# Performance work log

Hardware: AMD Instinct MI355X
Metric: run time of the kernel (lower is better)

The kernel has to match this reference:

```python
import jax, jax.numpy as jnp
import numpy as np

B, S, P, N, V = 8, 16, 32, 2048, 2562
K_SAMPLE = 500      # samples_per_slot
K_NEAREST = 3
MIN_DIST = 0.5
FALLOFF = 5.0
GW, SW, RW = 0.7, 0.3, 0.2


def _icosphere(level=4):
    t = (1.0 + 5.0 ** 0.5) / 2.0
    v = np.array([[-1, t, 0], [1, t, 0], [-1, -t, 0], [1, -t, 0],
                  [0, -1, t], [0, 1, t], [0, -1, -t], [0, 1, -t],
                  [t, 0, -1], [t, 0, 1], [-t, 0, -1], [-t, 0, 1]], dtype=np.float64)
    v /= np.linalg.norm(v, axis=1, keepdims=True)
    f = [[0, 11, 5], [0, 5, 1], [0, 1, 7], [0, 7, 10], [0, 10, 11],
         [1, 5, 9], [5, 11, 4], [11, 10, 2], [10, 7, 6], [7, 1, 8],
         [3, 9, 4], [3, 4, 2], [3, 2, 6], [3, 6, 8], [3, 8, 9],
         [4, 9, 5], [2, 4, 11], [6, 2, 10], [8, 6, 7], [9, 8, 1]]
    verts = [x for x in v]
    for _ in range(level):
        cache = {}
        def mid(a, b):
            key = (min(a, b), max(a, b))
            if key in cache:
                return cache[key]
            m = verts[a] + verts[b]
            m = m / np.linalg.norm(m)
            verts.append(m)
            cache[key] = len(verts) - 1
            return cache[key]
        nf = []
        for a, b, c in f:
            ab, bc, ca = mid(a, b), mid(b, c), mid(c, a)
            nf += [[a, ab, ca], [b, bc, ab], [c, ca, bc], [ab, bc, ca]]
        f = nf
    return np.asarray(verts, dtype=np.float32)


def _euler_xyz_to_matrix(ang):
    # pytorch3d euler_angles_to_matrix(..., 'XYZ'): R = Rx(a) @ Ry(b) @ Rz(c)
    a, b, c = ang[..., 0], ang[..., 1], ang[..., 2]
    ca, sa = jnp.cos(a), jnp.sin(a)
    cb, sb = jnp.cos(b), jnp.sin(b)
    cc, sc = jnp.cos(c), jnp.sin(c)
    o, z = jnp.ones_like(a), jnp.zeros_like(a)
    sh = ang.shape[:-1] + (3, 3)
    Rx = jnp.stack([o, z, z, z, ca, -sa, z, sa, ca], -1).reshape(sh)
    Ry = jnp.stack([cb, z, sb, z, o, z, -sb, z, cb], -1).reshape(sh)
    Rz = jnp.stack([cc, -sc, z, sc, cc, z, z, z, o], -1).reshape(sh)
    return Rx @ Ry @ Rz


def _cdist2(x, y):
    # squared euclidean distances: x [..., n, 3], y [..., m, 3] -> [..., n, m]
    x2 = (x * x).sum(-1)[..., :, None]
    y2 = (y * y).sum(-1)[..., None, :]
    return jnp.maximum(x2 + y2 - 2.0 * jnp.einsum('...nd,...md->...nm', x, y), 0.0)


def _forward(scales, transforms, prototype_weights, prototype_offsets, target_pcl, verts):
    # --- transform_mesh ---
    R = _euler_xyz_to_matrix(transforms[..., 3:])          # [B,S,P,3,3]
    deformed = verts[None] + prototype_offsets              # [P,V,3]
    rotated = jnp.einsum('pvj,bspij->bspvi', deformed, R)   # verts @ R^T
    scaled = rotated * scales[:, :, None, None, :]          # [B,S,P,V,3]
    translated = scaled + transforms[:, :, :, None, :3]
    final = jnp.einsum('bspvi,bsp->bsvi', translated, prototype_weights)  # [B,S,V,3]

    # --- hybrid chamfer loss ---
    pred = final[:, :, :K_SAMPLE, :]                        # deterministic per-slot samples
    pred_flat = pred.reshape(B, S * K_SAMPLE, 3)
    # global: target -> all predicted points, mean of K nearest squared dists
    d2g = _cdist2(target_pcl, pred_flat)                    # [B,N,S*K]
    knn = -jax.lax.top_k(-d2g, K_NEAREST)[0]
    global_loss = knn.mean()
    # per-slot: each slot's points -> target, nearest neighbor squared dist
    d2s = _cdist2(pred, target_pcl[:, None])                # [B,S,K,N]
    per_slot_loss = d2s.min(-1).mean()
    # centroid repulsion
    cent = final.mean(axis=2)                               # [B,S,3]
    eye = jnp.eye(S, dtype=final.dtype)
    d = jnp.sqrt(_cdist2(cent, cent) + eye)                 # eye keeps diag grads finite
    rep = jnp.exp(FALLOFF * jnp.maximum(MIN_DIST - d, 0.0)) * (1.0 - eye)
    rep_loss = (rep.sum(axis=(1, 2)) / (S * (S - 1))).mean()

    return GW * global_loss + SW * per_slot_loss + RW * rep_loss


def setup_inputs() -> dict:
    key = jax.random.key(0)
    ks = jax.random.split(key, 5)
    scales = jax.random.uniform(ks[0], (B, S, 1), jnp.float32) * 0.5 + 0.5
    transforms = jax.random.normal(ks[1], (B, S, P, 6), jnp.float32)
    w = jax.random.uniform(ks[2], (B, S, P), jnp.float32) + 1e-3
    prototype_weights = w / w.sum(-1, keepdims=True)
    prototype_offsets = jax.random.normal(ks[3], (P, V, 3), jnp.float32) * 0.1
    target_pcl = jax.random.normal(ks[4], (B, N, 3), jnp.float32)
    verts = jnp.asarray(_icosphere(4))                      # [2562,3]
    return {"scales": scales, "transforms": transforms,
            "prototype_weights": prototype_weights,
            "prototype_offsets": prototype_offsets,
            "target_pcl": target_pcl, "verts": verts}


def reference(scales, transforms, prototype_weights, prototype_offsets, target_pcl, verts):
    return _forward(scales, transforms, prototype_weights, prototype_offsets, target_pcl, verts)
```

## Files before the change

### kernel.cpp

```cpp
#include <hip/hip_runtime.h>
#include <math.h>

namespace {
constexpr int cB = 8, cS = 16, cP = 32, cN = 2048, cV = 2562;
constexpr int cK = 500;
constexpr int cJ = cS * cK;
constexpr int cJC = 16;
constexpr int cJCH = cJ / cJC;
constexpr int cNC = 8;
constexpr int cNCH = cN / cNC;
constexpr int cJPAD = 8192;
constexpr int cBN = cB * cN;
constexpr float FINF = 3.402823466e+38f;

constexpr int OFF_PRED4 = 0;
constexpr int OFF_TGT4  = 256000;
constexpr int OFF_VBAR  = 321536;
constexpr int OFF_OBAR  = 321540;
constexpr int OFF_SM    = 321664;
constexpr int OFF_SC    = 358528;
constexpr int OFF_T3    = 358912;
constexpr int OFF_PSP   = 1145344;
constexpr int OFF_GM    = 1669632;
constexpr int OFF_PS    = 1669696;
}

__device__ __forceinline__ float block_sum(float v, float* red, int tid) {
  red[tid] = v;
  __syncthreads();
  for (int s = 128; s > 0; s >>= 1) {
    if (tid < s) red[tid] += red[tid + s];
    __syncthreads();
  }
  return red[0];
}

__device__ __forceinline__ void top3_insert(float& t0, float& t1, float& t2, float d) {
  const float nt2 = fminf(t2, fmaxf(t1, d));
  const float nt1 = __builtin_amdgcn_fmed3f(t0, t1, d);
  t0 = fminf(t0, d);
  t1 = nt1;
  t2 = nt2;
}

__global__ void __launch_bounds__(256) k_front(const float* __restrict__ scales,
                                               const float* __restrict__ transforms,
                                               const float* __restrict__ pw,
                                               const float* __restrict__ offs,
                                               const float* __restrict__ verts,
                                               const float* __restrict__ target,
                                               float* __restrict__ ws) {
  const int blk = blockIdx.x;
  const int tid = threadIdx.x;
  if (blk <= cP) {
    __shared__ float red[256];
    const float* src = (blk < cP) ? (offs + blk * cV * 3) : verts;
    float acc0 = 0.f, acc1 = 0.f, acc2 = 0.f;
    for (int v = tid; v < cV; v += 256) {
      acc0 += src[v * 3 + 0];
      acc1 += src[v * 3 + 1];
      acc2 += src[v * 3 + 2];
    }
    float* dst = (blk < cP) ? (ws + OFF_OBAR + blk * 3) : (ws + OFF_VBAR);
    float a[3] = {acc0, acc1, acc2};
    for (int c = 0; c < 3; ++c) {
      float s = block_sum(a[c], red, tid);
      if (tid == 0) dst[c] = s / (float)cV;
      __syncthreads();
    }
  } else if (blk <= cP + 64) {
    const int idx = (blk - (cP + 1)) * 256 + tid;
    const float x = target[idx * 3 + 0];
    const float y = target[idx * 3 + 1];
    const float z = target[idx * 3 + 2];
    ((float4*)(ws + OFF_TGT4))[idx] =
        make_float4(x, y, z, 0.5f * fmaf(x, x, fmaf(y, y, z * z)));
  } else {
    const int bs = blk - (cP + 65);
    __shared__ float sM[cP][9];
    __shared__ float sC[3];
    __shared__ float sWT[cP][3];
    if (tid < cP) {
      const int p = tid;
      const float* t = transforms + (bs * cP + p) * 6;
      const float w = pw[bs * cP + p];
      const float sc = scales[bs];
      const float a = t[3], b = t[4], c = t[5];
      const float ca = cosf(a), sa = sinf(a);
      const float cb = cosf(b), sb = sinf(b);
      const float cg = cosf(c), sg = sinf(c);
      const float f = w * sc;
      sM[p][0] = f * (cb * cg);
      sM[p][1] = f * (-cb * sg);
      sM[p][2] = f * (sb);
      sM[p][3] = f * (ca * sg + sa * sb * cg);
      sM[p][4] = f * (ca * cg - sa * sb * sg);
      sM[p][5] = f * (-sa * cb);
      sM[p][6] = f * (sa * sg - ca * sb * cg);
      sM[p][7] = f * (sa * cg + ca * sb * sg);
      sM[p][8] = f * (ca * cb);
      sWT[p][0] = w * t[0];
      sWT[p][1] = w * t[1];
      sWT[p][2] = w * t[2];
    }
    __syncthreads();
    if (tid < 3) {
      float s = 0.f;
      for (int p = 0; p < cP; ++p) s += sWT[p][tid];
      sC[tid] = s;
    }
    __syncthreads();
    if (tid < cP * 9) ws[OFF_SM + bs * 288 + tid] = ((const float*)sM)[tid];
    if (tid < 3) ws[OFF_SC + bs * 3 + tid] = sC[tid];
    for (int k = tid; k < cK; k += 256) {
      const float x0 = verts[k * 3 + 0], x1 = verts[k * 3 + 1], x2 = verts[k * 3 + 2];
      float a0 = sC[0], a1 = sC[1], a2 = sC[2];
#pragma unroll 8
      for (int p = 0; p < cP; ++p) {
        const float* o = offs + (p * cV + k) * 3;
        const float d0 = x0 + o[0], d1 = x1 + o[1], d2 = x2 + o[2];
        a0 = fmaf(sM[p][0], d0, fmaf(sM[p][1], d1, fmaf(sM[p][2], d2, a0)));
        a1 = fmaf(sM[p][3], d0, fmaf(sM[p][4], d1, fmaf(sM[p][5], d2, a1)));
        a2 = fmaf(sM[p][6], d0, fmaf(sM[p][7], d1, fmaf(sM[p][8], d2, a2)));
      }
      ((float4*)(ws + OFF_PRED4))[bs * cK + k] =
          make_float4(a0, a1, a2, 0.5f * fmaf(a0, a0, fmaf(a1, a1, a2 * a2)));
    }
  }
}

__global__ void __launch_bounds__(256) k_global(float* __restrict__ ws) {
  __shared__ float4 sP[cJCH];
  const int nb = blockIdx.x, jc = blockIdx.y, b = blockIdx.z;
  const int tid = threadIdx.x;
  const float4* pr = (const float4*)(ws + OFF_PRED4) + b * cJ + jc * cJCH;
  for (int i = tid; i < cJCH; i += 256) sP[i] = pr[i];
  __syncthreads();
  const int n = nb * 256 + tid;
  const float4* tg = (const float4*)(ws + OFF_TGT4) + b * cN;
  const float4 tA = tg[n];
  const float4 tB = tg[n + 1024];
  float a0 = FINF, a1 = FINF, a2 = FINF;
  float b0 = FINF, b1 = FINF, b2 = FINF;
#pragma unroll 4
  for (int j = 0; j < cJCH; ++j) {
    const float4 p = sP[j];
    const float sA = fmaf(-tA.x, p.x, fmaf(-tA.y, p.y, fmaf(-tA.z, p.z, p.w)));
    const float sB = fmaf(-tB.x, p.x, fmaf(-tB.y, p.y, fmaf(-tB.z, p.z, p.w)));
    top3_insert(a0, a1, a2, sA);
    top3_insert(b0, b1, b2, sB);
  }
  float* plane = ws + OFF_T3 + (jc * 3) * cBN;
  const int idxA = b * cN + n;
  plane[0 * cBN + idxA] = a0;
  plane[1 * cBN + idxA] = a1;
  plane[2 * cBN + idxA] = a2;
  plane[0 * cBN + idxA + 1024] = b0;
  plane[1 * cBN + idxA + 1024] = b1;
  plane[2 * cBN + idxA + 1024] = b2;
}

__global__ void __launch_bounds__(256) k_perslot(float* __restrict__ ws) {
  __shared__ float4 sT[cNCH];
  const int jb = blockIdx.x;
  const int nc = blockIdx.y;
  const int b = blockIdx.z;
  const int tid = threadIdx.x;
  const float4* tg = (const float4*)(ws + OFF_TGT4) + b * cN + nc * cNCH;
  sT[tid] = tg[tid];
  __syncthreads();
  const float4* pr = (const float4*)(ws + OFF_PRED4) + b * cJ;
  float px[4], py[4], pz[4];
  float m[4] = {FINF, FINF, FINF, FINF};
#pragma unroll
  for (int q = 0; q < 4; ++q) {
    int j = jb * 1024 + q * 256 + tid;
    j = (j < cJ) ? j : (cJ - 1);
    const float4 p = pr[j];
    px[q] = p.x; py[q] = p.y; pz[q] = p.z;
  }
#pragma unroll 2
  for (int n = 0; n < cNCH; ++n) {
    const float4 t = sT[n];
#pragma unroll
    for (int q = 0; q < 4; ++q) {
      const float s = fmaf(-px[q], t.x, fmaf(-py[q], t.y, fmaf(-pz[q], t.z, t.w)));
      m[q] = fminf(m[q], s);
    }
  }
  float* o = ws + OFF_PSP + (b * cNC + nc) * cJPAD + jb * 1024 + tid;
#pragma unroll
  for (int q = 0; q < 4; ++q) o[q * 256] = m[q];
}

__global__ void __launch_bounds__(256) k_merge(float* __restrict__ ws) {
  __shared__ float red[256];
  const int blk = blockIdx.x;
  const int tid = threadIdx.x;
  if (blk < 64) {
    const int idx = blk * 256 + tid;
    const float* plane = ws + OFF_T3;
    float t0 = FINF, t1 = FINF, t2 = FINF;
#pragma unroll
    for (int q = 0; q < cJC * 3; ++q)
      top3_insert(t0, t1, t2, plane[q * cBN + idx]);
    const float ht = ws[OFF_TGT4 + idx * 4 + 3];
    const float d0 = fmaxf(2.f * (t0 + ht), 0.f);
    const float d1 = fmaxf(2.f * (t1 + ht), 0.f);
    const float d2 = fmaxf(2.f * (t2 + ht), 0.f);
    const float s = block_sum(d0 + d1 + d2, red, tid);
    if (tid == 0) ws[OFF_GM + blk] = s;
  } else {
    const int rb = blk - 64;
    const int b = rb >> 5;
    const int jb = rb & 31;
    const int j = jb * 256 + tid;
    float contrib = 0.f;
    if (j < cJ) {
      float m = FINF;
#pragma unroll
      for (int nc = 0; nc < cNC; ++nc)
        m = fminf(m, ws[OFF_PSP + (b * cNC + nc) * cJPAD + j]);
      const float hp = ws[OFF_PRED4 + (b * cJ + j) * 4 + 3];
      contrib = fmaxf(2.f * (m + hp), 0.f);
    }
    const float s = block_sum(contrib, red, tid);
    if (tid == 0) ws[OFF_PS + b * 32 + jb] = s;
  }
}

__global__ void __launch_bounds__(256) k_final(float* __restrict__ ws, float* __restrict__ out) {
  __shared__ float red[256];
  __shared__ float scent[cB * cS * 3];
  const int tid = threadIdx.x;
  if (tid < cB * cS) {
    const int bs = tid;
    const float* M = ws + OFF_SM + bs * 288;
    const float* vb = ws + OFF_VBAR;
    float c0 = ws[OFF_SC + bs * 3 + 0];
    float c1 = ws[OFF_SC + bs * 3 + 1];
    float c2 = ws[OFF_SC + bs * 3 + 2];
#pragma unroll 8
    for (int p = 0; p < cP; ++p) {
      const float* ob = ws + OFF_OBAR + p * 3;
      const float d0 = vb[0] + ob[0], d1 = vb[1] + ob[1], d2 = vb[2] + ob[2];
      c0 = fmaf(M[p * 9 + 0], d0, fmaf(M[p * 9 + 1], d1, fmaf(M[p * 9 + 2], d2, c0)));
      c1 = fmaf(M[p * 9 + 3], d0, fmaf(M[p * 9 + 4], d1, fmaf(M[p * 9 + 5], d2, c1)));
      c2 = fmaf(M[p * 9 + 6], d0, fmaf(M[p * 9 + 7], d1, fmaf(M[p * 9 + 8], d2, c2)));
    }
    scent[bs * 3 + 0] = c0;
    scent[bs * 3 + 1] = c1;
    scent[bs * 3 + 2] = c2;
  }
  __syncthreads();
  float acc = 0.f;
  for (int idx = tid; idx < cB * cS * cS; idx += 256) {
    const int b = idx / (cS * cS);
    const int r = idx % (cS * cS);
    const int i = r / cS, jj = r % cS;
    if (i == jj) continue;
    const float* ci = scent + (b * cS + i) * 3;
    const float* cj = scent + (b * cS + jj) * 3;
    const float dx = ci[0] - cj[0], dy = ci[1] - cj[1], dz = ci[2] - cj[2];
    const float d = sqrtf(fmaf(dx, dx, fmaf(dy, dy, dz * dz)));
    acc += expf(5.0f * fmaxf(0.5f - d, 0.0f));
  }
  const float repsum = block_sum(acc, red, tid);
  __syncthreads();
  const float gsum = block_sum((tid < 64) ? ws[OFF_GM + tid] : 0.f, red, tid);
  __syncthreads();
  const float pssum = block_sum(ws[OFF_PS + tid], red, tid);
  if (tid == 0) {
    const float global_loss = gsum / (float)(cB * cN * 3);
    const float per_slot = pssum / (float)(cB * cS * cK);
    const float rep = repsum / (float)(cB * cS * (cS - 1));
    out[0] = 0.7f * global_loss + 0.3f * per_slot + 0.2f * rep;
  }
}

extern "C" void kernel_launch(void* const* d_in, const int* in_sizes, int n_in,
                              void* d_out, int out_size, void* d_ws, size_t ws_size,
                              hipStream_t stream) {
  const float* scales     = (const float*)d_in[0];
  const float* transforms = (const float*)d_in[1];
  const float* pw         = (const float*)d_in[2];
  const float* offs       = (const float*)d_in[3];
  const float* target     = (const float*)d_in[4];
  const float* verts      = (const float*)d_in[5];
  float* out = (float*)d_out;
  float* ws = (float*)d_ws;

  k_front<<<cP + 1 + 64 + cB * cS, 256, 0, stream>>>(scales, transforms, pw, offs,
                                                     verts, target, ws);
  k_global<<<dim3(cN / 512, cJC, cB), 256, 0, stream>>>(ws);
  k_perslot<<<dim3(cJPAD / 1024, cNC, cB), 256, 0, stream>>>(ws);
  k_merge<<<64 + 256, 256, 0, stream>>>(ws);
  k_final<<<1, 256, 0, stream>>>(ws, out);
}
```

Measured before the change: 68.30 us.

## Fuse global and per-slot distance kernels into one launch with more register blocking

```diff
diff --git a/kernel.cpp b/kernel.cpp
--- a/kernel.cpp
+++ b/kernel.cpp
@@ -7,7 +7,7 @@
 constexpr int cJ = cS * cK;
 constexpr int cJC = 16;
 constexpr int cJCH = cJ / cJC;
-constexpr int cNC = 8;
+constexpr int cNC = 16;
 constexpr int cNCH = cN / cNC;
 constexpr int cJPAD = 8192;
 constexpr int cBN = cB * cN;
@@ -21,8 +21,8 @@
 constexpr int OFF_SC    = 358528;
 constexpr int OFF_T3    = 358912;
 constexpr int OFF_PSP   = 1145344;
-constexpr int OFF_GM    = 1669632;
-constexpr int OFF_PS    = 1669696;
+constexpr int OFF_GM    = 2193920;
+constexpr int OFF_PS    = 2193984;
 }
 
 __device__ __forceinline__ float block_sum(float v, float* red, int tid) {
@@ -36,11 +36,11 @@
 }
 
 __device__ __forceinline__ void top3_insert(float& t0, float& t1, float& t2, float d) {
-  const float nt2 = fminf(t2, fmaxf(t1, d));
-  const float nt1 = __builtin_amdgcn_fmed3f(t0, t1, d);
+  const float n1 = __builtin_amdgcn_fmed3f(t0, t1, d);
+  const float n2 = __builtin_amdgcn_fmed3f(t1, t2, d);
   t0 = fminf(t0, d);
-  t1 = nt1;
-  t2 = nt2;
+  t1 = n1;
+  t2 = n2;
 }
 
 __global__ void __launch_bounds__(256) k_front(const float* __restrict__ scales,
@@ -129,68 +129,84 @@
   }
 }
 
-__global__ void __launch_bounds__(256) k_global(float* __restrict__ ws) {
-  __shared__ float4 sP[cJCH];
-  const int nb = blockIdx.x, jc = blockIdx.y, b = blockIdx.z;
+__global__ void __launch_bounds__(256) k_dist(float* __restrict__ ws) {
+  __shared__ float4 sBuf[cJCH];
+  const int blk = blockIdx.x;
   const int tid = threadIdx.x;
-  const float4* pr = (const float4*)(ws + OFF_PRED4) + b * cJ + jc * cJCH;
-  for (int i = tid; i < cJCH; i += 256) sP[i] = pr[i];
-  __syncthreads();
-  const int n = nb * 256 + tid;
-  const float4* tg = (const float4*)(ws + OFF_TGT4) + b * cN;
-  const float4 tA = tg[n];
-  const float4 tB = tg[n + 1024];
-  float a0 = FINF, a1 = FINF, a2 = FINF;
-  float b0 = FINF, b1 = FINF, b2 = FINF;
-#pragma unroll 4
-  for (int j = 0; j < cJCH; ++j) {
-    const float4 p = sP[j];
-    const float sA = fmaf(-tA.x, p.x, fmaf(-tA.y, p.y, fmaf(-tA.z, p.z, p.w)));
-    const float sB = fmaf(-tB.x, p.x, fmaf(-tB.y, p.y, fmaf(-tB.z, p.z, p.w)));
-    top3_insert(a0, a1, a2, sA);
-    top3_insert(b0, b1, b2, sB);
-  }
-  float* plane = ws + OFF_T3 + (jc * 3) * cBN;
-  const int idxA = b * cN + n;
-  plane[0 * cBN + idxA] = a0;
-  plane[1 * cBN + idxA] = a1;
-  plane[2 * cBN + idxA] = a2;
-  plane[0 * cBN + idxA + 1024] = b0;
-  plane[1 * cBN + idxA + 1024] = b1;
-  plane[2 * cBN + idxA + 1024] = b2;
-}
-
-__global__ void __launch_bounds__(256) k_perslot(float* __restrict__ ws) {
-  __shared__ float4 sT[cNCH];
-  const int jb = blockIdx.x;
-  const int nc = blockIdx.y;
-  const int b = blockIdx.z;
-  const int tid = threadIdx.x;
-  const float4* tg = (const float4*)(ws + OFF_TGT4) + b * cN + nc * cNCH;
-  sT[tid] = tg[tid];
-  __syncthreads();
-  const float4* pr = (const float4*)(ws + OFF_PRED4) + b * cJ;
-  float px[4], py[4], pz[4];
-  float m[4] = {FINF, FINF, FINF, FINF};
-#pragma unroll
-  for (int q = 0; q < 4; ++q) {
-    int j = jb * 1024 + q * 256 + tid;
-    j = (j < cJ) ? j : (cJ - 1);
-    const float4 p = pr[j];
-    px[q] = p.x; py[q] = p.y; pz[q] = p.z;
-  }
+  if (blk < 256) {
+    const int nb = blk & 1;
+    const int jc = (blk >> 1) & 15;
+    const int b = blk >> 5;
+    const float4* pr = (const float4*)(ws + OFF_PRED4) + b * cJ + jc * cJCH;
+    for (int i = tid; i < cJCH; i += 256) sBuf[i] = pr[i];
+    __syncthreads();
+    const int n0 = nb * 1024 + tid;
+    const float4* tg = (const float4*)(ws + OFF_TGT4) + b * cN;
+    const float4 tA = tg[n0];
+    const float4 tB = tg[n0 + 256];
+    const float4 tC = tg[n0 + 512];
+    const float4 tD = tg[n0 + 768];
+    float a0 = FINF, a1 = FINF, a2 = FINF;
+    float b0 = FINF, b1 = FINF, b2 = FINF;
+    float c0 = FINF, c1 = FINF, c2 = FINF;
+    float d0 = FINF, d1 = FINF, d2 = FINF;
 #pragma unroll 2
-  for (int n = 0; n < cNCH; ++n) {
-    const float4 t = sT[n];
-#pragma unroll
-    for (int q = 0; q < 4; ++q) {
-      const float s = fmaf(-px[q], t.x, fmaf(-py[q], t.y, fmaf(-pz[q], t.z, t.w)));
-      m[q] = fminf(m[q], s);
-    }
-  }
-  float* o = ws + OFF_PSP + (b * cNC + nc) * cJPAD + jb * 1024 + tid;
-#pragma unroll
-  for (int q = 0; q < 4; ++q) o[q * 256] = m[q];
+    for (int j = 0; j < cJCH; ++j) {
+      const float4 p = sBuf[j];
+      const float sA = fmaf(-tA.x, p.x, fmaf(-tA.y, p.y, fmaf(-tA.z, p.z, p.w)));
+      const float sB = fmaf(-tB.x, p.x, fmaf(-tB.y, p.y, fmaf(-tB.z, p.z, p.w)));
+      const float sC_ = fmaf(-tC.x, p.x, fmaf(-tC.y, p.y, fmaf(-tC.z, p.z, p.w)));
+      const float sD = fmaf(-tD.x, p.x, fmaf(-tD.y, p.y, fmaf(-tD.z, p.z, p.w)));
+      top3_insert(a0, a1, a2, sA);
+      top3_insert(b0, b1, b2, sB);
+      top3_insert(c0, c1, c2, sC_);
+      top3_insert(d0, d1, d2, sD);
+    }
+    float* plane = ws + OFF_T3 + (jc * 3) * cBN;
+    const int idx = b * cN + n0;
+    plane[0 * cBN + idx] = a0;
+    plane[1 * cBN + idx] = a1;
+    plane[2 * cBN + idx] = a2;
+    plane[0 * cBN + idx + 256] = b0;
+    plane[1 * cBN + idx + 256] = b1;
+    plane[2 * cBN + idx + 256] = b2;
+    plane[0 * cBN + idx + 512] = c0;
+    plane[1 * cBN + idx + 512] = c1;
+    plane[2 * cBN + idx + 512] = c2;
+    plane[0 * cBN + idx + 768] = d0;
+    plane[1 * cBN + idx + 768] = d1;
+    plane[2 * cBN + idx + 768] = d2;
+  } else {
+    const int rb = blk - 256;
+    const int jb = rb & 3;
+    const int nc = (rb >> 2) & 15;
+    const int b = rb >> 6;
+    const float4* tg = (const float4*)(ws + OFF_TGT4) + b * cN + nc * cNCH;
+    if (tid < cNCH) sBuf[tid] = tg[tid];
+    __syncthreads();
+    const float4* pr = (const float4*)(ws + OFF_PRED4) + b * cJ;
+    float px[8], py[8], pz[8];
+    float m[8] = {FINF, FINF, FINF, FINF, FINF, FINF, FINF, FINF};
+#pragma unroll
+    for (int q = 0; q < 8; ++q) {
+      int j = jb * 2048 + q * 256 + tid;
+      j = (j < cJ) ? j : (cJ - 1);
+      const float4 p = pr[j];
+      px[q] = p.x; py[q] = p.y; pz[q] = p.z;
+    }
+#pragma unroll 2
+    for (int n = 0; n < cNCH; ++n) {
+      const float4 t = sBuf[n];
+#pragma unroll
+      for (int q = 0; q < 8; ++q) {
+        const float s = fmaf(-px[q], t.x, fmaf(-py[q], t.y, fmaf(-pz[q], t.z, t.w)));
+        m[q] = fminf(m[q], s);
+      }
+    }
+    float* o = ws + OFF_PSP + (b * cNC + nc) * cJPAD + jb * 2048 + tid;
+#pragma unroll
+    for (int q = 0; q < 8; ++q) o[q * 256] = m[q];
+  }
 }
 
 __global__ void __launch_bounds__(256) k_merge(float* __restrict__ ws) {
@@ -292,8 +308,7 @@
 
   k_front<<<cP + 1 + 64 + cB * cS, 256, 0, stream>>>(scales, transforms, pw, offs,
                                                      verts, target, ws);
-  k_global<<<dim3(cN / 512, cJC, cB), 256, 0, stream>>>(ws);
-  k_perslot<<<dim3(cJPAD / 1024, cNC, cB), 256, 0, stream>>>(ws);
+  k_dist<<<768, 256, 0, stream>>>(ws);
   k_merge<<<64 + 256, 256, 0, stream>>>(ws);
   k_final<<<1, 256, 0, stream>>>(ws, out);
 }
```

Result: faster. 66.46 us (-2.7%).
